# Kernel tuning notes

Hardware: AMD Instinct MI355X
Metric: run time of the kernel (lower is better)

## Reference

```python
import jax, jax.numpy as jnp
import numpy as np

B, D_IN, N, L, P, C = 512, 784, 2048, 6, 15, 10  # batch, input, width, dag layers, weight pairs, classes


def setup_inputs() -> dict:
    key = jax.random.key(0)
    ks = jax.random.split(key, 10)
    x = jax.random.normal(ks[0], (B, D_IN), jnp.float32)
    w_in = jax.random.normal(ks[1], (N, D_IN), jnp.float32) * 0.1
    b_in = jax.random.normal(ks[2], (N,), jnp.float32) * 0.1
    W = jax.random.normal(ks[3], (P, N, N), jnp.float32) * 0.1
    # binary 0/1 float masks standing in for DAG connectivity masks
    M = jax.random.bernoulli(ks[4], 0.5, (P, N, N)).astype(jnp.float32)
    b = jax.random.normal(ks[5], (L - 1, N), jnp.float32) * 0.1
    w_out1 = jax.random.normal(ks[6], (C, N), jnp.float32) * 0.1
    b_out1 = jax.random.normal(ks[7], (C,), jnp.float32) * 0.1
    w_out2 = jax.random.normal(ks[8], (C, N), jnp.float32) * 0.1
    b_out2 = jax.random.normal(ks[9], (C,), jnp.float32) * 0.1
    return {"x": x, "w_in": w_in, "b_in": b_in, "W": W, "M": M, "b": b,
            "w_out1": w_out1, "b_out1": b_out1, "w_out2": w_out2, "b_out2": b_out2}


def reference(x, w_in, b_in, W, M, b, w_out1, b_out1, w_out2, b_out2):
    # input layer
    acts = [jax.nn.relu(x @ w_in.T + b_in)]  # [B, N]
    idx = 0
    for i in range(1, L):  # DAG layer i has predecessors 0..i-1
        Wm = W[idx:idx + i] * M[idx:idx + i]          # [i, N, N] masked weights
        stacked = jnp.stack(acts)                      # [i, B, N]
        # sum over predecessors of inp @ Wm.T; bias added once per predecessor
        out = jnp.einsum('jbn,jmn->bm', stacked, Wm) + i * b[i - 1]
        acts.append(jax.nn.relu(out))
        idx += i
    return acts[-1] @ w_out1.T + b_out1 + acts[-2] @ w_out2.T + b_out2
```

## Files before the change

### kernel.cpp

```cpp
#include <hip/hip_runtime.h>

typedef __bf16 bf16;
typedef __attribute__((ext_vector_type(8))) __bf16 bf16x8;
typedef __attribute__((ext_vector_type(4))) __bf16 bf16x4;
typedef __attribute__((ext_vector_type(4))) float floatx4;

#define B_SZ 512
#define N_SZ 2048
#define DIN  784
#define DINP 800
#define ACT_LD 12288

__device__ __forceinline__ void load_lds16(const bf16* g, bf16* l) {
    __builtin_amdgcn_global_load_lds(
        (const __attribute__((address_space(1))) void*)g,
        (__attribute__((address_space(3))) void*)l, 16, 0, 0);
}

__global__ __launch_bounds__(256)
void prep_kernel(const float* __restrict__ x, const float* __restrict__ w_in,
                 bf16* __restrict__ xb, bf16* __restrict__ w_inb)
{
    int g = blockIdx.x * 256 + threadIdx.x;
    const int GPR = DINP / 4;
    const float* src; bf16* dst; int row, c;
    if (g < B_SZ * GPR) {
        row = g / GPR; c = g - row * GPR;
        src = x + (size_t)row * DIN;  dst = xb + (size_t)row * DINP;
    } else {
        int h = g - B_SZ * GPR;
        row = h / GPR; c = h - row * GPR;
        src = w_in + (size_t)row * DIN;  dst = w_inb + (size_t)row * DINP;
    }
    int k = c * 4;
    floatx4 v = (floatx4){0.f, 0.f, 0.f, 0.f};
    if (k < DIN) v = *(const floatx4*)(src + k);
    bf16x4 o;
    o[0] = (bf16)v[0]; o[1] = (bf16)v[1]; o[2] = (bf16)v[2]; o[3] = (bf16)v[3];
    *(bf16x4*)(dst + k) = o;
}

__global__ __launch_bounds__(256, 2)
void gemm_kernel(const bf16* __restrict__ A, int lda,
                 const bf16* __restrict__ Bm, int ldb,
                 float* __restrict__ partial,
                 int chunkK, int Ktot)
{
    __shared__ bf16 As[128 * 32];
    __shared__ bf16 Bs[128 * 32];

    const int t    = threadIdx.x;
    const int lane = t & 63, wave = t >> 6;
    const int wm   = (wave & 1) * 64, wn = (wave >> 1) * 64;
    const int l15  = lane & 15, quad = lane >> 4;
    const int n0   = blockIdx.x * 128, m0 = blockIdx.y * 128;
    const int s    = blockIdx.z;
    const int kb   = s * chunkK;
    const int ke   = (kb + chunkK < Ktot) ? (kb + chunkK) : Ktot;

    const int rA = wave * 16 + (lane >> 2);
    const int cA = (lane & 3) * 8;
    const bf16* pA0 = A  + (size_t)(m0 + rA) * lda + cA + kb;
    const bf16* pA1 = pA0 + (size_t)64 * lda;
    const bf16* pB0 = Bm + (size_t)(n0 + rA) * ldb + cA + kb;
    const bf16* pB1 = pB0 + (size_t)64 * ldb;
    bf16* dA0 = &As[wave * 512];  bf16* dA1 = &As[(wave + 4) * 512];
    bf16* dB0 = &Bs[wave * 512];  bf16* dB1 = &Bs[(wave + 4) * 512];

    floatx4 acc[4][4];
#pragma unroll
    for (int a = 0; a < 4; a++)
#pragma unroll
        for (int b = 0; b < 4; b++) acc[a][b] = (floatx4){0.f, 0.f, 0.f, 0.f};

    for (int k0 = kb; k0 < ke; k0 += 32) {
        __syncthreads();
        load_lds16(pA0, dA0);  load_lds16(pA1, dA1);
        load_lds16(pB0, dB0);  load_lds16(pB1, dB1);
        pA0 += 32; pA1 += 32; pB0 += 32; pB1 += 32;
        __syncthreads();

        bf16x8 af[4], bfr[4];
#pragma unroll
        for (int a = 0; a < 4; a++)
            af[a] = *(const bf16x8*)(&As[(wm + a * 16 + l15) * 32 + quad * 8]);
#pragma unroll
        for (int b = 0; b < 4; b++)
            bfr[b] = *(const bf16x8*)(&Bs[(wn + b * 16 + l15) * 32 + quad * 8]);
#pragma unroll
        for (int a = 0; a < 4; a++)
#pragma unroll
            for (int b = 0; b < 4; b++)
                acc[a][b] = __builtin_amdgcn_mfma_f32_16x16x32_bf16(af[a], bfr[b], acc[a][b], 0, 0, 0);
    }

    float* outp = partial + (size_t)s * (B_SZ * N_SZ);
#pragma unroll
    for (int a = 0; a < 4; a++)
#pragma unroll
        for (int b = 0; b < 4; b++)
#pragma unroll
            for (int r = 0; r < 4; r++) {
                int row = m0 + wm + a * 16 + quad * 4 + r;
                int col = n0 + wn + b * 16 + l15;
                outp[(size_t)row * N_SZ + col] = acc[a][b][r];
            }
}

__global__ __launch_bounds__(256, 2)
void dag_gemm_kernel(const bf16* __restrict__ A,
                     const float* __restrict__ Wl, const float* __restrict__ Ml,
                     float* __restrict__ partial,
                     int chunkK)
{
    __shared__ bf16 As[2][256 * 32];
    __shared__ bf16 Bs[2][64 * 32];

    const int t    = threadIdx.x;
    const int lane = t & 63, wave = t >> 6;
    const int l15  = lane & 15, quad = lane >> 4;
    const int n0   = blockIdx.x * 64, m0 = blockIdx.y * 256;
    const int kb   = blockIdx.z * chunkK;
    const int ke   = kb + chunkK;

    const int ar = wave * 16 + (lane >> 2);
    const int ac = (lane & 3) * 8;
    const int br = t >> 2, bc = (t & 3) * 8;
    const size_t wrow = (size_t)(n0 + br) << 11;

    floatx4 acc[4][4];
#pragma unroll
    for (int a = 0; a < 4; a++)
#pragma unroll
        for (int b = 0; b < 4; b++) acc[a][b] = (floatx4){0.f, 0.f, 0.f, 0.f};

    bf16x8 a0, a1, a2, a3;
    floatx4 wv0, wv1, mv0, mv1;

    auto load_regs = [&](int k) {
        const bf16* ap = A + (size_t)(m0 + ar) * ACT_LD + k + ac;
        a0 = *(const bf16x8*)(ap);
        a1 = *(const bf16x8*)(ap + (size_t)64  * ACT_LD);
        a2 = *(const bf16x8*)(ap + (size_t)128 * ACT_LD);
        a3 = *(const bf16x8*)(ap + (size_t)192 * ACT_LD);
        int jj = k >> 11, kk = k & 2047;
        size_t o = ((size_t)jj << 22) + wrow + kk + bc;
        wv0 = *(const floatx4*)(Wl + o);  wv1 = *(const floatx4*)(Wl + o + 4);
        mv0 = *(const floatx4*)(Ml + o);  mv1 = *(const floatx4*)(Ml + o + 4);
    };

    auto do_step = [&](int buf, int knext, bool pref) {
        bf16x8 o8;
        o8[0] = (bf16)(wv0[0] * mv0[0]); o8[1] = (bf16)(wv0[1] * mv0[1]);
        o8[2] = (bf16)(wv0[2] * mv0[2]); o8[3] = (bf16)(wv0[3] * mv0[3]);
        o8[4] = (bf16)(wv1[0] * mv1[0]); o8[5] = (bf16)(wv1[1] * mv1[1]);
        o8[6] = (bf16)(wv1[2] * mv1[2]); o8[7] = (bf16)(wv1[3] * mv1[3]);
        *(bf16x8*)(&Bs[buf][br * 32 + bc]) = o8;
        *(bf16x8*)(&As[buf][(ar +   0) * 32 + ac]) = a0;
        *(bf16x8*)(&As[buf][(ar +  64) * 32 + ac]) = a1;
        *(bf16x8*)(&As[buf][(ar + 128) * 32 + ac]) = a2;
        *(bf16x8*)(&As[buf][(ar + 192) * 32 + ac]) = a3;
        if (pref) load_regs(knext);
        __syncthreads();
        bf16x8 af[4], bfr[4];
#pragma unroll
        for (int a = 0; a < 4; a++)
            af[a] = *(const bf16x8*)(&As[buf][(wave * 64 + a * 16 + l15) * 32 + quad * 8]);
#pragma unroll
        for (int b = 0; b < 4; b++)
            bfr[b] = *(const bf16x8*)(&Bs[buf][(b * 16 + l15) * 32 + quad * 8]);
#pragma unroll
        for (int a = 0; a < 4; a++)
#pragma unroll
            for (int b = 0; b < 4; b++)
                acc[a][b] = __builtin_amdgcn_mfma_f32_16x16x32_bf16(af[a], bfr[b], acc[a][b], 0, 0, 0);
    };

    load_regs(kb);
    for (int k0 = kb; k0 < ke; k0 += 64) {
        do_step(0, k0 + 32, true);
        do_step(1, k0 + 64, (k0 + 64) < ke);
    }

    float* outp = partial + (size_t)blockIdx.z * (B_SZ * N_SZ);
#pragma unroll
    for (int a = 0; a < 4; a++)
#pragma unroll
        for (int b = 0; b < 4; b++)
#pragma unroll
            for (int r = 0; r < 4; r++) {
                int row = m0 + wave * 64 + a * 16 + quad * 4 + r;
                int col = n0 + b * 16 + l15;
                outp[(size_t)row * N_SZ + col] = acc[a][b][r];
            }
}

__global__ __launch_bounds__(256)
void epilogue_kernel(const float* __restrict__ partial, int S,
                     const float* __restrict__ bias, float bscale,
                     bf16* __restrict__ actdst)
{
    int g = blockIdx.x * 256 + threadIdx.x;
    size_t off = (size_t)g * 4;
    int b = (int)(off >> 11);
    int n = (int)(off & (N_SZ - 1));
    floatx4 v = *(const floatx4*)(partial + off);
    for (int s2 = 1; s2 < S; s2++)
        v += *(const floatx4*)(partial + (size_t)s2 * (B_SZ * N_SZ) + off);
    floatx4 bv = *(const floatx4*)(bias + n);
    bf16x4 o;
#pragma unroll
    for (int j = 0; j < 4; j++) {
        float xv = v[j] + bscale * bv[j];
        xv = xv > 0.f ? xv : 0.f;
        o[j] = (bf16)xv;
    }
    *(bf16x4*)(actdst + (size_t)b * ACT_LD + n) = o;
}

__global__ __launch_bounds__(64)
void out_kernel(const bf16* __restrict__ act4, const bf16* __restrict__ act5,
                const float* __restrict__ w1, const float* __restrict__ b1,
                const float* __restrict__ w2, const float* __restrict__ b2,
                float* __restrict__ out)
{
    int b = blockIdx.x, lane = threadIdx.x;
    float a5[32], a4[32];
#pragma unroll
    for (int rep = 0; rep < 4; rep++) {
        bf16x8 v5 = *(const bf16x8*)(act5 + (size_t)b * ACT_LD + rep * 512 + lane * 8);
        bf16x8 v4 = *(const bf16x8*)(act4 + (size_t)b * ACT_LD + rep * 512 + lane * 8);
#pragma unroll
        for (int j = 0; j < 8; j++) {
            a5[rep * 8 + j] = (float)v5[j];
            a4[rep * 8 + j] = (float)v4[j];
        }
    }
    for (int c = 0; c < 10; c++) {
        float d = 0.f;
#pragma unroll
        for (int rep = 0; rep < 4; rep++) {
            floatx4 wa = *(const floatx4*)(w1 + (size_t)c * N_SZ + rep * 512 + lane * 8);
            floatx4 wb = *(const floatx4*)(w1 + (size_t)c * N_SZ + rep * 512 + lane * 8 + 4);
            floatx4 va = *(const floatx4*)(w2 + (size_t)c * N_SZ + rep * 512 + lane * 8);
            floatx4 vb = *(const floatx4*)(w2 + (size_t)c * N_SZ + rep * 512 + lane * 8 + 4);
#pragma unroll
            for (int j = 0; j < 4; j++) {
                d += a5[rep * 8 + j] * wa[j] + a4[rep * 8 + j] * va[j];
                d += a5[rep * 8 + 4 + j] * wb[j] + a4[rep * 8 + 4 + j] * vb[j];
            }
        }
        for (int off = 32; off > 0; off >>= 1) d += __shfl_down(d, off);
        if (lane == 0) out[b * 10 + c] = d + b1[c] + b2[c];
    }
}

extern "C" void kernel_launch(void* const* d_in, const int* in_sizes, int n_in,
                              void* d_out, int out_size, void* d_ws, size_t ws_size,
                              hipStream_t stream)
{
    const float* x    = (const float*)d_in[0];
    const float* w_in = (const float*)d_in[1];
    const float* b_in = (const float*)d_in[2];
    const float* W    = (const float*)d_in[3];
    const float* M    = (const float*)d_in[4];
    const float* bL   = (const float*)d_in[5];
    const float* w1   = (const float*)d_in[6];
    const float* b1   = (const float*)d_in[7];
    const float* w2   = (const float*)d_in[8];
    const float* b2   = (const float*)d_in[9];
    float* out = (float*)d_out;

    char* ws = (char*)d_ws;
    bf16*  xb      = (bf16*)ws;
    bf16*  w_inb   = (bf16*)(ws + 819200);
    bf16*  actsT   = (bf16*)(ws + 4096000);
    float* partial = (float*)(ws + 16678912);

    prep_kernel<<<2000, 256, 0, stream>>>(x, w_in, xb, w_inb);

    gemm_kernel<<<dim3(16, 4, 4), 256, 0, stream>>>(
        xb, DINP, w_inb, DINP, partial, 224, DINP);
    epilogue_kernel<<<1024, 256, 0, stream>>>(partial, 4, b_in, 1.0f, actsT);

    for (int i = 1; i < 6; i++) {
        int idx = i * (i - 1) / 2;
        const float* Wl = W + ((size_t)idx << 22);
        const float* Ml = M + ((size_t)idx << 22);
        dag_gemm_kernel<<<dim3(32, 2, 8), 256, 0, stream>>>(
            actsT, Wl, Ml, partial, 256 * i);
        epilogue_kernel<<<1024, 256, 0, stream>>>(
            partial, 8, bL + (size_t)(i - 1) * N_SZ, (float)i,
            actsT + (size_t)i * N_SZ);
    }

    out_kernel<<<512, 64, 0, stream>>>(
        actsT + (size_t)4 * N_SZ, actsT + (size_t)5 * N_SZ,
        w1, b1, w2, b2, out);
}
```

Measured before the change: 690.9 us.

## Cover full batch per block, read activations directly from global, swizzle LDS

The DAG GEMM kernel now uses 512-thread blocks that each cover all 512 batch rows for a 64-column tile. W and M for that tile are streamed once rather than twice, since the previous grid split the batch into two 256-row halves. Activation fragments are loaded straight from global/L2 into registers instead of being staged through LDS, and the masked-weight LDS tile uses a 64-wide K step with an XOR swizzle and deeper register prefetch. The grid is flattened so split-K chunks of the same column tile are adjacent. The risks are uncoalesced direct A loads that depend on cache hits, and higher register pressure at 512 threads.

```diff
diff --git a/kernel.cpp b/kernel.cpp
--- a/kernel.cpp
+++ b/kernel.cpp
@@ -107,26 +107,27 @@
             }
 }
 
-__global__ __launch_bounds__(256, 2)
+__global__ __launch_bounds__(512, 2)
 void dag_gemm_kernel(const bf16* __restrict__ A,
                      const float* __restrict__ Wl, const float* __restrict__ Ml,
                      float* __restrict__ partial,
                      int chunkK)
 {
-    __shared__ bf16 As[2][256 * 32];
-    __shared__ bf16 Bs[2][64 * 32];
+    __shared__ bf16 Bs[2][64 * 64];
 
     const int t    = threadIdx.x;
     const int lane = t & 63, wave = t >> 6;
     const int l15  = lane & 15, quad = lane >> 4;
-    const int n0   = blockIdx.x * 64, m0 = blockIdx.y * 256;
-    const int kb   = blockIdx.z * chunkK;
+    const int n0   = (blockIdx.x >> 3) * 64;
+    const int z    = blockIdx.x & 7;
+    const int kb   = z * chunkK;
     const int ke   = kb + chunkK;
 
-    const int ar = wave * 16 + (lane >> 2);
-    const int ac = (lane & 3) * 8;
-    const int br = t >> 2, bc = (t & 3) * 8;
+    const int br = t >> 3, bc = (t & 7) * 8;
     const size_t wrow = (size_t)(n0 + br) << 11;
+    bf16* bdst = &Bs[0][br * 64 + (bc ^ ((br & 7) << 3))];
+
+    const bf16* Abase = A + (size_t)(wave * 64 + l15) * ACT_LD + quad * 8;
 
     floatx4 acc[4][4];
 #pragma unroll
@@ -134,62 +135,82 @@
 #pragma unroll
         for (int b = 0; b < 4; b++) acc[a][b] = (floatx4){0.f, 0.f, 0.f, 0.f};
 
-    bf16x8 a0, a1, a2, a3;
-    floatx4 wv0, wv1, mv0, mv1;
-
-    auto load_regs = [&](int k) {
-        const bf16* ap = A + (size_t)(m0 + ar) * ACT_LD + k + ac;
-        a0 = *(const bf16x8*)(ap);
-        a1 = *(const bf16x8*)(ap + (size_t)64  * ACT_LD);
-        a2 = *(const bf16x8*)(ap + (size_t)128 * ACT_LD);
-        a3 = *(const bf16x8*)(ap + (size_t)192 * ACT_LD);
-        int jj = k >> 11, kk = k & 2047;
-        size_t o = ((size_t)jj << 22) + wrow + kk + bc;
-        wv0 = *(const floatx4*)(Wl + o);  wv1 = *(const floatx4*)(Wl + o + 4);
-        mv0 = *(const floatx4*)(Ml + o);  mv1 = *(const floatx4*)(Ml + o + 4);
+    floatx4 w0a, w1a, m0a, m1a;
+    floatx4 w0b, w1b, m0b, m1b;
+
+#define LOAD_WM(k, w0, w1, m0, m1) do {                          \
+        int jj = (k) >> 11, kk2 = (k) & 2047;                     \
+        size_t o = ((size_t)jj << 22) + wrow + kk2 + bc;          \
+        w0 = *(const floatx4*)(Wl + o);                           \
+        w1 = *(const floatx4*)(Wl + o + 4);                       \
+        m0 = *(const floatx4*)(Ml + o);                           \
+        m1 = *(const floatx4*)(Ml + o + 4);                       \
+    } while (0)
+
+#define PACK(buf, w0, w1, m0, m1) do {                           \
+        bf16x8 o8;                                                \
+        o8[0] = (bf16)(w0[0] * m0[0]); o8[1] = (bf16)(w0[1] * m0[1]); \
+        o8[2] = (bf16)(w0[2] * m0[2]); o8[3] = (bf16)(w0[3] * m0[3]); \
+        o8[4] = (bf16)(w1[0] * m1[0]); o8[5] = (bf16)(w1[1] * m1[1]); \
+        o8[6] = (bf16)(w1[2] * m1[2]); o8[7] = (bf16)(w1[3] * m1[3]); \
+        *(bf16x8*)(bdst + (buf) * 4096) = o8;                     \
+    } while (0)
+
+    auto compute = [&](int buf, int k0) {
+        bf16x8 af[8];
+        const bf16* ap = Abase + k0;
+#pragma unroll
+        for (int a = 0; a < 4; a++) {
+            af[a]     = *(const bf16x8*)(ap + (size_t)(a * 16) * ACT_LD);
+            af[4 + a] = *(const bf16x8*)(ap + (size_t)(a * 16) * ACT_LD + 32);
+        }
+#pragma unroll
+        for (int kk = 0; kk < 2; kk++) {
+            bf16x8 bfr[4];
+#pragma unroll
+            for (int b = 0; b < 4; b++) {
+                int r = b * 16 + l15;
+                int e = (kk * 32 + quad * 8) ^ ((r & 7) << 3);
+                bfr[b] = *(const bf16x8*)(&Bs[buf][r * 64 + e]);
+            }
+#pragma unroll
+            for (int a = 0; a < 4; a++)
+#pragma unroll
+                for (int b = 0; b < 4; b++)
+                    acc[a][b] = __builtin_amdgcn_mfma_f32_16x16x32_bf16(
+                        af[kk * 4 + a], bfr[b], acc[a][b], 0, 0, 0);
+        }
     };
 
-    auto do_step = [&](int buf, int knext, bool pref) {
-        bf16x8 o8;
-        o8[0] = (bf16)(wv0[0] * mv0[0]); o8[1] = (bf16)(wv0[1] * mv0[1]);
-        o8[2] = (bf16)(wv0[2] * mv0[2]); o8[3] = (bf16)(wv0[3] * mv0[3]);
-        o8[4] = (bf16)(wv1[0] * mv1[0]); o8[5] = (bf16)(wv1[1] * mv1[1]);
-        o8[6] = (bf16)(wv1[2] * mv1[2]); o8[7] = (bf16)(wv1[3] * mv1[3]);
-        *(bf16x8*)(&Bs[buf][br * 32 + bc]) = o8;
-        *(bf16x8*)(&As[buf][(ar +   0) * 32 + ac]) = a0;
-        *(bf16x8*)(&As[buf][(ar +  64) * 32 + ac]) = a1;
-        *(bf16x8*)(&As[buf][(ar + 128) * 32 + ac]) = a2;
-        *(bf16x8*)(&As[buf][(ar + 192) * 32 + ac]) = a3;
-        if (pref) load_regs(knext);
+    LOAD_WM(kb,       w0a, w1a, m0a, m1a);
+    LOAD_WM(kb + 64,  w0b, w1b, m0b, m1b);
+    PACK(0, w0a, w1a, m0a, m1a);
+    LOAD_WM(kb + 128, w0a, w1a, m0a, m1a);
+    __syncthreads();
+
+    const int nt = chunkK >> 6;
+    for (int tt = 0; tt < nt; tt += 2) {
+        const int k0 = kb + tt * 64;
+        compute(0, k0);
+        PACK(1, w0b, w1b, m0b, m1b);
+        if (k0 + 192 < ke) LOAD_WM(k0 + 192, w0b, w1b, m0b, m1b);
         __syncthreads();
-        bf16x8 af[4], bfr[4];
-#pragma unroll
-        for (int a = 0; a < 4; a++)
-            af[a] = *(const bf16x8*)(&As[buf][(wave * 64 + a * 16 + l15) * 32 + quad * 8]);
+        compute(1, k0 + 64);
+        PACK(0, w0a, w1a, m0a, m1a);
+        if (k0 + 256 < ke) LOAD_WM(k0 + 256, w0a, w1a, m0a, m1a);
+        __syncthreads();
+    }
+#undef LOAD_WM
+#undef PACK
+
+    float* outp = partial + (size_t)z * (B_SZ * N_SZ);
+#pragma unroll
+    for (int a = 0; a < 4; a++)
 #pragma unroll
         for (int b = 0; b < 4; b++)
-            bfr[b] = *(const bf16x8*)(&Bs[buf][(b * 16 + l15) * 32 + quad * 8]);
-#pragma unroll
-        for (int a = 0; a < 4; a++)
-#pragma unroll
-            for (int b = 0; b < 4; b++)
-                acc[a][b] = __builtin_amdgcn_mfma_f32_16x16x32_bf16(af[a], bfr[b], acc[a][b], 0, 0, 0);
-    };
-
-    load_regs(kb);
-    for (int k0 = kb; k0 < ke; k0 += 64) {
-        do_step(0, k0 + 32, true);
-        do_step(1, k0 + 64, (k0 + 64) < ke);
-    }
-
-    float* outp = partial + (size_t)blockIdx.z * (B_SZ * N_SZ);
-#pragma unroll
-    for (int a = 0; a < 4; a++)
-#pragma unroll
-        for (int b = 0; b < 4; b++)
 #pragma unroll
             for (int r = 0; r < 4; r++) {
-                int row = m0 + wave * 64 + a * 16 + quad * 4 + r;
+                int row = wave * 64 + a * 16 + quad * 4 + r;
                 int col = n0 + b * 16 + l15;
                 outp[(size_t)row * N_SZ + col] = acc[a][b][r];
             }
@@ -287,7 +308,7 @@
         int idx = i * (i - 1) / 2;
         const float* Wl = W + ((size_t)idx << 22);
         const float* Ml = M + ((size_t)idx << 22);
-        dag_gemm_kernel<<<dim3(32, 2, 8), 256, 0, stream>>>(
+        dag_gemm_kernel<<<256, 512, 0, stream>>>(
             actsT, Wl, Ml, partial, 256 * i);
         epilogue_kernel<<<1024, 256, 0, stream>>>(
             partial, 8, bL + (size_t)(i - 1) * N_SZ, (float)i,
```

Result: faster. 661.8 us (-4.2%).
